# Optimization experiments

Measured on AMD Instinct MI355X. Metric: run time of the kernel, lower is better.

## Reference

```python
import jax, jax.numpy as jnp
import numpy as np

D_K = 64

def setup_inputs() -> dict:
    key = jax.random.key(0)
    kq, kk, kv = jax.random.split(key, 3)
    B, Lq, Lk, d = 32, 2048, 2048, D_K
    return {
        "query": jax.random.normal(kq, (B, Lq, d), dtype=jnp.float32),
        "key": jax.random.normal(kk, (B, Lk, d), dtype=jnp.float32),
        "value": jax.random.normal(kv, (B, Lk, d), dtype=jnp.float32),
    }

def reference(query, key, value):
    d_k = query.shape[-1]
    scale = 1.0 / jnp.sqrt(jnp.asarray(d_k, query.dtype))
    scores = jnp.einsum('nqd,nkd->nqk', query, key) * scale  # (B, Lq, Lk)
    attn = jax.nn.softmax(scores, axis=-1)  # masked=None -> plain softmax; dropout p=0.0 is identity
    return jnp.einsum('nqk,nkd->nqd', attn, value)  # (B, Lq, d_v)
```

## Files before the change

### kernel.cpp

```cpp
#include <hip/hip_runtime.h>


#define NB   32
#define LSEQ 2048
#define DH   64
#define BM   64
#define BN   64
#define NIT  (LSEQ / BN)

typedef __attribute__((ext_vector_type(8)))  __bf16 bf16x8;
typedef __attribute__((ext_vector_type(16))) float  f32x16;

union BF8 { bf16x8 v; unsigned short u[8]; unsigned u32[4]; uint4 q; };

__device__ __forceinline__ unsigned short f2bf(float f) {
    unsigned int u = __builtin_bit_cast(unsigned int, f);
    u += 0x7fffu + ((u >> 16) & 1u);
    return (unsigned short)(u >> 16);
}

__device__ __forceinline__ unsigned pack_bf2(float a, float b) {
    unsigned ua = __builtin_bit_cast(unsigned, a) + 0x8000u;
    unsigned ub = __builtin_bit_cast(unsigned, b) + 0x8000u;
    return __builtin_amdgcn_perm(ub, ua, 0x07060302u);
}

__device__ __forceinline__ float fast_exp2(float x) {
#if __has_builtin(__builtin_amdgcn_exp2f)
    return __builtin_amdgcn_exp2f(x);
#else
    return exp2f(x);
#endif
}

__device__ __forceinline__ void load_lds16(const void* g, void* l) {
    __builtin_amdgcn_global_load_lds(
        (const __attribute__((address_space(1))) void*)g,
        (__attribute__((address_space(3))) void*)l, 16, 0, 0);
}

#define KBLK ((NB * LSEQ * 8) / 256)
__global__ __launch_bounds__(256)
void prep(const float* __restrict__ Kg, const float* __restrict__ Vg,
          unsigned short* __restrict__ Kb, unsigned short* __restrict__ Vt) {
    __shared__ unsigned short T[64 * 65];
    const int tid = threadIdx.x;
    if (blockIdx.x < KBLK) {
        const int CH  = blockIdx.x * 256 + tid;
        const int b   = CH >> 14;
        const int rem = CH & 16383;
        const int n   = rem >> 3;
        const int cc  = rem & 7;
        const int c   = cc ^ (n & 7);
        const float* src = Kg + (((size_t)b * LSEQ + n) * DH + c * 8);
        float4 f0 = ((const float4*)src)[0];
        float4 f1 = ((const float4*)src)[1];
        BF8 t;
        t.u[0]=f2bf(f0.x); t.u[1]=f2bf(f0.y); t.u[2]=f2bf(f0.z); t.u[3]=f2bf(f0.w);
        t.u[4]=f2bf(f1.x); t.u[5]=f2bf(f1.y); t.u[6]=f2bf(f1.z); t.u[7]=f2bf(f1.w);
        *(bf16x8*)&Kb[(size_t)CH * 8] = t.v;
    } else {
        const int bx = blockIdx.x - KBLK;
        const int b  = bx >> 5;
        const int nt = bx & 31;
        const int nl = tid >> 2;
        const int dc = (tid & 3) * 16;
        const float* src = Vg + (((size_t)b * LSEQ + nt * 64 + nl) * DH + dc);
        float4 f0 = ((const float4*)src)[0];
        float4 f1 = ((const float4*)src)[1];
        float4 f2 = ((const float4*)src)[2];
        float4 f3 = ((const float4*)src)[3];
        float vv[16] = {f0.x,f0.y,f0.z,f0.w, f1.x,f1.y,f1.z,f1.w,
                        f2.x,f2.y,f2.z,f2.w, f3.x,f3.y,f3.z,f3.w};
        #pragma unroll
        for (int i = 0; i < 16; ++i)
            T[(dc + i) * 65 + nl] = f2bf(vv[i]);
        __syncthreads();
        #pragma unroll
        for (int i = 0; i < 2; ++i) {
            const int CH = i * 256 + tid;
            const int d  = CH >> 3;
            const int cc = CH & 7;
            const int nloc = (cc ^ (d & 7)) * 8;
            BF8 o;
            #pragma unroll
            for (int j = 0; j < 8; ++j) o.u[j] = T[d * 65 + nloc + j];
            *(bf16x8*)&Vt[(((size_t)(b * 64 + d)) * 256 + nt * 8 + cc) * 8] = o.v;
        }
    }
}

__global__ __launch_bounds__(256, 4)
void attn_fwd(const unsigned short* __restrict__ Kb,
              const unsigned short* __restrict__ Vt,
              const float* __restrict__ Qg,
              float* __restrict__ Og) {
    __shared__ __align__(16) char smem[32768];
    unsigned short* Kl = (unsigned short*)smem;
    unsigned short* Vl = (unsigned short*)(smem + 16384);
    float* Mrg = (float*)smem;
    float* Lsh = (float*)(smem + 18432);

    const int tid  = threadIdx.x;
    const int wave = tid >> 6;
    const int lane = tid & 63;
    const int m32  = lane & 31;
    const int h    = lane >> 5;
    const int qh   = wave >> 1;
    const int kvh  = wave & 1;
    const int b    = blockIdx.y;
    const int qt   = blockIdx.x;

    const float qscale = 0.18033688011112042f;
    const int qrow = qt * BM + qh * 32 + m32;
    bf16x8 qf[4];
    {
        const float* qp = Qg + ((size_t)(b * LSEQ + qrow)) * DH;
        #pragma unroll
        for (int kt = 0; kt < 4; ++kt) {
            const float* p4 = qp + kt * 16 + h * 8;
            float4 f0 = ((const float4*)p4)[0];
            float4 f1 = ((const float4*)p4)[1];
            BF8 t;
            t.u[0]=f2bf(f0.x*qscale); t.u[1]=f2bf(f0.y*qscale);
            t.u[2]=f2bf(f0.z*qscale); t.u[3]=f2bf(f0.w*qscale);
            t.u[4]=f2bf(f1.x*qscale); t.u[5]=f2bf(f1.y*qscale);
            t.u[6]=f2bf(f1.z*qscale); t.u[7]=f2bf(f1.w*qscale);
            qf[kt] = t.v;
        }
    }

    int kidx[4];
    #pragma unroll
    for (int kt = 0; kt < 4; ++kt) {
        const int n  = kvh * 32 + m32;
        const int cc = kt * 2 + h;
        kidx[kt] = (n * 8 + (cc ^ (n & 7))) * 8;
    }
    int vidx[2][2];
    #pragma unroll
    for (int dt = 0; dt < 2; ++dt)
        #pragma unroll
        for (int kt = 0; kt < 2; ++kt) {
            const int d  = dt * 32 + m32;
            const int cc = kvh * 4 + kt * 2 + h;
            vidx[dt][kt] = (d * 8 + (cc ^ (d & 7))) * 8;
        }

    const char* kgb = (const char*)Kb + (size_t)b * (LSEQ * DH * 2);
    const char* vgb = (const char*)Vt + (size_t)b * (DH * LSEQ * 2);
    const int CH0 = wave * 128 + lane;
    const int CH1 = CH0 + 64;
    const int voff0 = (CH0 >> 3) * (LSEQ * 2) + (CH0 & 7) * 16;
    const int voff1 = (CH1 >> 3) * (LSEQ * 2) + (CH1 & 7) * 16;

    {
        char* kd = smem + wave * 2048;
        char* vd = smem + 16384 + wave * 2048;
        load_lds16(kgb + CH0 * 16, kd);
        load_lds16(kgb + CH1 * 16, kd + 1024);
        load_lds16(vgb + voff0, vd);
        load_lds16(vgb + voff1, vd + 1024);
    }

    f32x16 o0, o1;
    #pragma unroll
    for (int i = 0; i < 16; ++i) { o0[i] = 0.f; o1[i] = 0.f; }
    float l_run = 0.f;

    for (int nt = 0; nt < NIT; ++nt) {
        const int cur = nt & 1;
        __syncthreads();

        if (nt + 1 < NIT) {
            char* kd = smem + (cur ^ 1) * 8192 + wave * 2048;
            char* vd = smem + 16384 + (cur ^ 1) * 8192 + wave * 2048;
            load_lds16(kgb + (nt + 1) * 8192 + CH0 * 16, kd);
            load_lds16(kgb + (nt + 1) * 8192 + CH1 * 16, kd + 1024);
            load_lds16(vgb + (nt + 1) * 128 + voff0, vd);
            load_lds16(vgb + (nt + 1) * 128 + voff1, vd + 1024);
        }

        const unsigned short* kb = Kl + cur * 4096;
        f32x16 s;
        #pragma unroll
        for (int i = 0; i < 16; ++i) s[i] = 0.f;
        #pragma unroll
        for (int kt = 0; kt < 4; ++kt) {
            bf16x8 kf = *(const bf16x8*)&kb[kidx[kt]];
            s = __builtin_amdgcn_mfma_f32_32x32x16_bf16(kf, qf[kt], s, 0, 0, 0);
        }

        const unsigned short* vb = Vl + cur * 4096;
        BF8 vf[2][2];
        #pragma unroll
        for (int dt = 0; dt < 2; ++dt)
            #pragma unroll
            for (int kt = 0; kt < 2; ++kt)
                vf[dt][kt].v = *(const bf16x8*)&vb[vidx[dt][kt]];

        float e[16];
        #pragma unroll
        for (int r = 0; r < 16; ++r) e[r] = fast_exp2(s[r]);
        #pragma unroll
        for (int g = 0; g < 4; ++g)
            l_run += ((e[4*g] + e[4*g+1]) + (e[4*g+2] + e[4*g+3]));
        unsigned pk[8];
        #pragma unroll
        for (int g = 0; g < 4; ++g) {
            pk[2*g]   = pack_bf2(e[4*g],   e[4*g+1]);
            pk[2*g+1] = pack_bf2(e[4*g+2], e[4*g+3]);
        }

        const unsigned sA0 = h ? pk[0] : pk[2];
        const unsigned sA1 = h ? pk[1] : pk[3];
        const unsigned sB0 = h ? pk[4] : pk[6];
        const unsigned sB1 = h ? pk[5] : pk[7];
        const unsigned rA0 = __shfl_xor((int)sA0, 32, 64);
        const unsigned rA1 = __shfl_xor((int)sA1, 32, 64);
        const unsigned rB0 = __shfl_xor((int)sB0, 32, 64);
        const unsigned rB1 = __shfl_xor((int)sB1, 32, 64);
        BF8 p0, p1;
        p0.u32[0] = h ? rA0 : pk[0];  p0.u32[1] = h ? rA1 : pk[1];
        p0.u32[2] = h ? pk[2] : rA0;  p0.u32[3] = h ? pk[3] : rA1;
        p1.u32[0] = h ? rB0 : pk[4];  p1.u32[1] = h ? rB1 : pk[5];
        p1.u32[2] = h ? pk[6] : rB0;  p1.u32[3] = h ? pk[7] : rB1;

        o0 = __builtin_amdgcn_mfma_f32_32x32x16_bf16(vf[0][0].v, p0.v, o0, 0, 0, 0);
        o0 = __builtin_amdgcn_mfma_f32_32x32x16_bf16(vf[0][1].v, p1.v, o0, 0, 0, 0);
        o1 = __builtin_amdgcn_mfma_f32_32x32x16_bf16(vf[1][0].v, p0.v, o1, 0, 0, 0);
        o1 = __builtin_amdgcn_mfma_f32_32x32x16_bf16(vf[1][1].v, p1.v, o1, 0, 0, 0);
    }

    const float l2 = l_run + __shfl_xor(l_run, 32, 64);
    __syncthreads();
    if (kvh) {
        float* mp = Mrg + ((size_t)qh * 64 + lane) * 36;
        #pragma unroll
        for (int g = 0; g < 4; ++g) {
            *(float4*)(mp + 4*g)      = (float4){o0[4*g], o0[4*g+1], o0[4*g+2], o0[4*g+3]};
            *(float4*)(mp + 16 + 4*g) = (float4){o1[4*g], o1[4*g+1], o1[4*g+2], o1[4*g+3]};
        }
        if (h == 0) Lsh[qh * 32 + m32] = l2;
    }
    __syncthreads();
    if (!kvh) {
        const float* mp = Mrg + ((size_t)qh * 64 + lane) * 36;
        #pragma unroll
        for (int g = 0; g < 4; ++g) {
            float4 a = *(const float4*)(mp + 4*g);
            float4 c = *(const float4*)(mp + 16 + 4*g);
            o0[4*g] += a.x; o0[4*g+1] += a.y; o0[4*g+2] += a.z; o0[4*g+3] += a.w;
            o1[4*g] += c.x; o1[4*g+1] += c.y; o1[4*g+2] += c.z; o1[4*g+3] += c.w;
        }
        const float inv = 1.0f / (l2 + Lsh[qh * 32 + m32]);
        float* op = Og + ((size_t)(b * LSEQ + qrow)) * DH;
        #pragma unroll
        for (int t = 0; t < 2; ++t)
            #pragma unroll
            for (int g = 0; g < 4; ++g) {
                float4 v;
                v.x = (t ? o1[4*g+0] : o0[4*g+0]) * inv;
                v.y = (t ? o1[4*g+1] : o0[4*g+1]) * inv;
                v.z = (t ? o1[4*g+2] : o0[4*g+2]) * inv;
                v.w = (t ? o1[4*g+3] : o0[4*g+3]) * inv;
                *(float4*)(op + t * 32 + g * 8 + h * 4) = v;
            }
    }
}

extern "C" void kernel_launch(void* const* d_in, const int* in_sizes, int n_in,
                              void* d_out, int out_size, void* d_ws, size_t ws_size,
                              hipStream_t stream) {
    const float* Q = (const float*)d_in[0];
    const float* K = (const float*)d_in[1];
    const float* V = (const float*)d_in[2];
    float* O = (float*)d_out;

    unsigned short* Kb = (unsigned short*)d_ws;
    unsigned short* Vt = (unsigned short*)d_ws + 4u * 1024u * 1024u;

    prep<<<dim3(KBLK + NB * (LSEQ / 64)), dim3(256), 0, stream>>>(K, V, Kb, Vt);
    attn_fwd<<<dim3(LSEQ / BM, NB), dim3(256), 0, stream>>>(Kb, Vt, Q, O);
}
```

Baseline: 140.5 us.

## Load V fragments directly from global, swizzle block order, use permlane32 swap

Changes the V pre-transposed layout so each lane can read its MFMA operand fragments straight from global memory, dropping the V LDS staging and shrinking shared memory for higher occupancy. Remaps block indices so consecutive workgroups span different batches/tiles, adds s_setprio around MFMA blocks, fuses exp/pack loops, and replaces the cross-half shuffles with permlane32_swap. The prep kernel's transpose packs two rows per 32-bit LDS word. The direct global V loads are not prefetched ahead, so their latency may be exposed in the loop.

```diff
diff --git a/kernel.cpp b/kernel.cpp
--- a/kernel.cpp
+++ b/kernel.cpp
@@ -10,6 +10,7 @@
 
 typedef __attribute__((ext_vector_type(8)))  __bf16 bf16x8;
 typedef __attribute__((ext_vector_type(16))) float  f32x16;
+typedef __attribute__((ext_vector_type(2)))  unsigned uint2v;
 
 union BF8 { bf16x8 v; unsigned short u[8]; unsigned u32[4]; uint4 q; };
 
@@ -43,7 +44,7 @@
 __global__ __launch_bounds__(256)
 void prep(const float* __restrict__ Kg, const float* __restrict__ Vg,
           unsigned short* __restrict__ Kb, unsigned short* __restrict__ Vt) {
-    __shared__ unsigned short T[64 * 65];
+    __shared__ __align__(16) unsigned T2[64 * 36];
     const int tid = threadIdx.x;
     if (blockIdx.x < KBLK) {
         const int CH  = blockIdx.x * 256 + tid;
@@ -63,29 +64,28 @@
         const int bx = blockIdx.x - KBLK;
         const int b  = bx >> 5;
         const int nt = bx & 31;
-        const int nl = tid >> 2;
-        const int dc = (tid & 3) * 16;
-        const float* src = Vg + (((size_t)b * LSEQ + nt * 64 + nl) * DH + dc);
-        float4 f0 = ((const float4*)src)[0];
-        float4 f1 = ((const float4*)src)[1];
-        float4 f2 = ((const float4*)src)[2];
-        float4 f3 = ((const float4*)src)[3];
-        float vv[16] = {f0.x,f0.y,f0.z,f0.w, f1.x,f1.y,f1.z,f1.w,
-                        f2.x,f2.y,f2.z,f2.w, f3.x,f3.y,f3.z,f3.w};
-        #pragma unroll
-        for (int i = 0; i < 16; ++i)
-            T[(dc + i) * 65 + nl] = f2bf(vv[i]);
+        const int n  = (tid >> 3) * 2;
+        const int dc = (tid & 7) * 8;
+        const float* s0 = Vg + (((size_t)b * LSEQ + nt * 64 + n) * DH + dc);
+        float4 a0 = ((const float4*)s0)[0];
+        float4 a1 = ((const float4*)s0)[1];
+        const float* s1 = s0 + DH;
+        float4 b0 = ((const float4*)s1)[0];
+        float4 b1 = ((const float4*)s1)[1];
+        float va[8] = {a0.x,a0.y,a0.z,a0.w, a1.x,a1.y,a1.z,a1.w};
+        float vb[8] = {b0.x,b0.y,b0.z,b0.w, b1.x,b1.y,b1.z,b1.w};
+        const int n2 = n >> 1;
+        #pragma unroll
+        for (int j = 0; j < 8; ++j)
+            T2[(dc + j) * 36 + n2] = (unsigned)f2bf(va[j]) | ((unsigned)f2bf(vb[j]) << 16);
         __syncthreads();
         #pragma unroll
         for (int i = 0; i < 2; ++i) {
             const int CH = i * 256 + tid;
-            const int d  = CH >> 3;
-            const int cc = CH & 7;
-            const int nloc = (cc ^ (d & 7)) * 8;
-            BF8 o;
-            #pragma unroll
-            for (int j = 0; j < 8; ++j) o.u[j] = T[d * 65 + nloc + j];
-            *(bf16x8*)&Vt[(((size_t)(b * 64 + d)) * 256 + nt * 8 + cc) * 8] = o.v;
+            const int cc = CH >> 6;
+            const int d  = CH & 63;
+            uint4 o = *(const uint4*)&T2[d * 36 + cc * 4];
+            *(uint4*)&Vt[((((size_t)(b * 32 + nt)) * 8 + cc) * 64 + d) * 8] = o;
         }
     }
 }
@@ -95,9 +95,8 @@
               const unsigned short* __restrict__ Vt,
               const float* __restrict__ Qg,
               float* __restrict__ Og) {
-    __shared__ __align__(16) char smem[32768];
+    __shared__ __align__(16) char smem[18944];
     unsigned short* Kl = (unsigned short*)smem;
-    unsigned short* Vl = (unsigned short*)(smem + 16384);
     float* Mrg = (float*)smem;
     float* Lsh = (float*)(smem + 18432);
 
@@ -108,8 +107,11 @@
     const int h    = lane >> 5;
     const int qh   = wave >> 1;
     const int kvh  = wave & 1;
-    const int b    = blockIdx.y;
-    const int qt   = blockIdx.x;
+
+    const int L  = blockIdx.y * 32 + blockIdx.x;
+    const int Lp = (L & 7) * 128 + (L >> 3);
+    const int b  = Lp >> 5;
+    const int qt = Lp & 31;
 
     const float qscale = 0.18033688011112042f;
     const int qrow = qt * BM + qh * 32 + m32;
@@ -137,30 +139,21 @@
         const int cc = kt * 2 + h;
         kidx[kt] = (n * 8 + (cc ^ (n & 7))) * 8;
     }
-    int vidx[2][2];
-    #pragma unroll
-    for (int dt = 0; dt < 2; ++dt)
-        #pragma unroll
-        for (int kt = 0; kt < 2; ++kt) {
-            const int d  = dt * 32 + m32;
-            const int cc = kvh * 4 + kt * 2 + h;
-            vidx[dt][kt] = (d * 8 + (cc ^ (d & 7))) * 8;
-        }
+
+    const char* vgb = (const char*)Vt + (size_t)b * (32 * 8 * 64 * 16);
+    const int v00 = (((kvh * 4 + 0 + h) * 64) +  0 + m32) * 16;
+    const int v01 = (((kvh * 4 + 2 + h) * 64) +  0 + m32) * 16;
+    const int v10 = (((kvh * 4 + 0 + h) * 64) + 32 + m32) * 16;
+    const int v11 = (((kvh * 4 + 2 + h) * 64) + 32 + m32) * 16;
 
     const char* kgb = (const char*)Kb + (size_t)b * (LSEQ * DH * 2);
-    const char* vgb = (const char*)Vt + (size_t)b * (DH * LSEQ * 2);
     const int CH0 = wave * 128 + lane;
     const int CH1 = CH0 + 64;
-    const int voff0 = (CH0 >> 3) * (LSEQ * 2) + (CH0 & 7) * 16;
-    const int voff1 = (CH1 >> 3) * (LSEQ * 2) + (CH1 & 7) * 16;
 
     {
         char* kd = smem + wave * 2048;
-        char* vd = smem + 16384 + wave * 2048;
         load_lds16(kgb + CH0 * 16, kd);
         load_lds16(kgb + CH1 * 16, kd + 1024);
-        load_lds16(vgb + voff0, vd);
-        load_lds16(vgb + voff1, vd + 1024);
     }
 
     f32x16 o0, o1;
@@ -172,64 +165,81 @@
         const int cur = nt & 1;
         __syncthreads();
 
+        BF8 vf00, vf01, vf10, vf11;
+        {
+            const char* vp = vgb + nt * 8192;
+            vf00.q = *(const uint4*)(vp + v00);
+            vf01.q = *(const uint4*)(vp + v01);
+            vf10.q = *(const uint4*)(vp + v10);
+            vf11.q = *(const uint4*)(vp + v11);
+        }
+
         if (nt + 1 < NIT) {
             char* kd = smem + (cur ^ 1) * 8192 + wave * 2048;
-            char* vd = smem + 16384 + (cur ^ 1) * 8192 + wave * 2048;
             load_lds16(kgb + (nt + 1) * 8192 + CH0 * 16, kd);
             load_lds16(kgb + (nt + 1) * 8192 + CH1 * 16, kd + 1024);
-            load_lds16(vgb + (nt + 1) * 128 + voff0, vd);
-            load_lds16(vgb + (nt + 1) * 128 + voff1, vd + 1024);
         }
 
         const unsigned short* kb = Kl + cur * 4096;
         f32x16 s;
         #pragma unroll
         for (int i = 0; i < 16; ++i) s[i] = 0.f;
+        __builtin_amdgcn_s_setprio(1);
         #pragma unroll
         for (int kt = 0; kt < 4; ++kt) {
             bf16x8 kf = *(const bf16x8*)&kb[kidx[kt]];
             s = __builtin_amdgcn_mfma_f32_32x32x16_bf16(kf, qf[kt], s, 0, 0, 0);
         }
-
-        const unsigned short* vb = Vl + cur * 4096;
-        BF8 vf[2][2];
-        #pragma unroll
-        for (int dt = 0; dt < 2; ++dt)
-            #pragma unroll
-            for (int kt = 0; kt < 2; ++kt)
-                vf[dt][kt].v = *(const bf16x8*)&vb[vidx[dt][kt]];
-
-        float e[16];
-        #pragma unroll
-        for (int r = 0; r < 16; ++r) e[r] = fast_exp2(s[r]);
-        #pragma unroll
-        for (int g = 0; g < 4; ++g)
-            l_run += ((e[4*g] + e[4*g+1]) + (e[4*g+2] + e[4*g+3]));
+        __builtin_amdgcn_s_setprio(0);
+
         unsigned pk[8];
         #pragma unroll
         for (int g = 0; g < 4; ++g) {
-            pk[2*g]   = pack_bf2(e[4*g],   e[4*g+1]);
-            pk[2*g+1] = pack_bf2(e[4*g+2], e[4*g+3]);
-        }
-
-        const unsigned sA0 = h ? pk[0] : pk[2];
-        const unsigned sA1 = h ? pk[1] : pk[3];
-        const unsigned sB0 = h ? pk[4] : pk[6];
-        const unsigned sB1 = h ? pk[5] : pk[7];
-        const unsigned rA0 = __shfl_xor((int)sA0, 32, 64);
-        const unsigned rA1 = __shfl_xor((int)sA1, 32, 64);
-        const unsigned rB0 = __shfl_xor((int)sB0, 32, 64);
-        const unsigned rB1 = __shfl_xor((int)sB1, 32, 64);
+            float e0 = fast_exp2(s[4*g]);
+            float e1 = fast_exp2(s[4*g+1]);
+            float e2 = fast_exp2(s[4*g+2]);
+            float e3 = fast_exp2(s[4*g+3]);
+            l_run += ((e0 + e1) + (e2 + e3));
+            pk[2*g]   = pack_bf2(e0, e1);
+            pk[2*g+1] = pack_bf2(e2, e3);
+        }
+
         BF8 p0, p1;
-        p0.u32[0] = h ? rA0 : pk[0];  p0.u32[1] = h ? rA1 : pk[1];
-        p0.u32[2] = h ? pk[2] : rA0;  p0.u32[3] = h ? pk[3] : rA1;
-        p1.u32[0] = h ? rB0 : pk[4];  p1.u32[1] = h ? rB1 : pk[5];
-        p1.u32[2] = h ? pk[6] : rB0;  p1.u32[3] = h ? pk[7] : rB1;
-
-        o0 = __builtin_amdgcn_mfma_f32_32x32x16_bf16(vf[0][0].v, p0.v, o0, 0, 0, 0);
-        o0 = __builtin_amdgcn_mfma_f32_32x32x16_bf16(vf[0][1].v, p1.v, o0, 0, 0, 0);
-        o1 = __builtin_amdgcn_mfma_f32_32x32x16_bf16(vf[1][0].v, p0.v, o1, 0, 0, 0);
-        o1 = __builtin_amdgcn_mfma_f32_32x32x16_bf16(vf[1][1].v, p1.v, o1, 0, 0, 0);
+#if __has_builtin(__builtin_amdgcn_permlane32_swap)
+        {
+            uint2v r;
+            r = __builtin_amdgcn_permlane32_swap(pk[0], pk[2], false, false);
+            p0.u32[0] = r[0]; p0.u32[2] = r[1];
+            r = __builtin_amdgcn_permlane32_swap(pk[1], pk[3], false, false);
+            p0.u32[1] = r[0]; p0.u32[3] = r[1];
+            r = __builtin_amdgcn_permlane32_swap(pk[4], pk[6], false, false);
+            p1.u32[0] = r[0]; p1.u32[2] = r[1];
+            r = __builtin_amdgcn_permlane32_swap(pk[5], pk[7], false, false);
+            p1.u32[1] = r[0]; p1.u32[3] = r[1];
+        }
+#else
+        {
+            const unsigned sA0 = h ? pk[0] : pk[2];
+            const unsigned sA1 = h ? pk[1] : pk[3];
+            const unsigned sB0 = h ? pk[4] : pk[6];
+            const unsigned sB1 = h ? pk[5] : pk[7];
+            const unsigned rA0 = __shfl_xor((int)sA0, 32, 64);
+            const unsigned rA1 = __shfl_xor((int)sA1, 32, 64);
+            const unsigned rB0 = __shfl_xor((int)sB0, 32, 64);
+            const unsigned rB1 = __shfl_xor((int)sB1, 32, 64);
+            p0.u32[0] = h ? rA0 : pk[0];  p0.u32[1] = h ? rA1 : pk[1];
+            p0.u32[2] = h ? pk[2] : rA0;  p0.u32[3] = h ? pk[3] : rA1;
+            p1.u32[0] = h ? rB0 : pk[4];  p1.u32[1] = h ? rB1 : pk[5];
+            p1.u32[2] = h ? pk[6] : rB0;  p1.u32[3] = h ? pk[7] : rB1;
+        }
+#endif
+
+        __builtin_amdgcn_s_setprio(1);
+        o0 = __builtin_amdgcn_mfma_f32_32x32x16_bf16(vf00.v, p0.v, o0, 0, 0, 0);
+        o0 = __builtin_amdgcn_mfma_f32_32x32x16_bf16(vf01.v, p1.v, o0, 0, 0, 0);
+        o1 = __builtin_amdgcn_mfma_f32_32x32x16_bf16(vf10.v, p0.v, o1, 0, 0, 0);
+        o1 = __builtin_amdgcn_mfma_f32_32x32x16_bf16(vf11.v, p1.v, o1, 0, 0, 0);
+        __builtin_amdgcn_s_setprio(0);
     }
 
     const float l2 = l_run + __shfl_xor(l_run, 32, 64);
```

After: 137.2 us. 1.02x faster.
